# Kernel optimization log

Measured on AMD Instinct MI355X. Metric: run time of the kernel, lower is better.

The kernel has to match this reference:

```python
import jax, jax.numpy as jnp
import numpy as np

B, F, L, K = 16384, 8, 16, 4
NH, HD = 4, 2  # nhead=4, head_dim=2 (d_model=8)
EPS = 1e-5


def _ln(x, g, b):
    m = x.mean(-1, keepdims=True)
    v = ((x - m) ** 2).mean(-1, keepdims=True)
    return g * (x - m) * jax.lax.rsqrt(v + EPS) + b


def _encoder(x, ipw, ipb, ow, ob, l1w, l1b, l2w, l2b, n1g, n1b, n2g, n2b):
    # x: [N, L, 8]; post-norm TransformerEncoderLayer, relu FFN, eval (dropout off)
    N, Ls, D = x.shape
    for i in range(3):
        qkv = x @ ipw[i].T + ipb[i]                       # [N,L,24]
        q, k, v = jnp.split(qkv, 3, axis=-1)
        q = q.reshape(N, Ls, NH, HD)
        k = k.reshape(N, Ls, NH, HD)
        v = v.reshape(N, Ls, NH, HD)
        s = jnp.einsum('nqhd,nkhd->nhqk', q, k) / np.float32(np.sqrt(HD))
        a = jax.nn.softmax(s, axis=-1)
        o = jnp.einsum('nhqk,nkhd->nqhd', a, v).reshape(N, Ls, D)
        o = o @ ow[i].T + ob[i]
        x = _ln(x + o, n1g[i], n1b[i])
        h = jax.nn.relu(x @ l1w[i].T + l1b[i]) @ l2w[i].T + l2b[i]
        x = _ln(x + h, n2g[i], n2b[i])
    return x


def _forward(cidxs, slots, gfeats, f2, f3, tab_c, tab_s, fw, fb, ipw, ipb, ow, ob,
             l1w, l1b, l2w, l2b, n1g, n1b, n2g, n2b, uw, ub, w1, b1, w2, b2):
    Bn, Fn, Ln, _ = gfeats.shape
    x = gfeats.reshape(Bn * Fn, Ln, 4) @ fw.T + fb        # emb_floor -> [B*F,L,8]
    x = _encoder(x, ipw, ipb, ow, ob, l1w, l1b, l2w, l2b, n1g, n1b, n2g, n2b)
    floors = x.sum(axis=1).reshape(Bn, Fn, 8)             # sum over units
    units = jax.nn.relu(floors @ uw.T + ub).sum(axis=1)   # emb_unit + sum over floors -> [B,16]
    f1f2 = jnp.concatenate([tab_c[cidxs], tab_s[slots], units, f2], axis=-1)  # [B,36]
    Kn = f3.shape[1]
    z = jnp.concatenate(
        [jnp.broadcast_to(f1f2[:, None, :], (Bn, Kn, f1f2.shape[-1])), f3], axis=-1
    ).reshape(Bn * Kn, 42)                                # repeat_interleave + hstack f3
    h = jax.nn.relu(z @ w1.T + b1)                        # ff_match (dropout off)
    y = (h @ w2.T + b2).reshape(-1)
    return y


def setup_inputs() -> dict:
    key = jax.random.key(0)
    ks = jax.random.split(key, 30)
    r = lambda k, shp: (jax.random.normal(k, shp) * 0.1).astype(jnp.float32)
    return dict(
        cidxs=jax.random.randint(ks[0], (B,), 0, 100000),
        slots=jax.random.randint(ks[1], (B,), 0, 48),
        gfeats=jax.random.normal(ks[2], (B, F, L, 4), jnp.float32),
        f2=jax.random.normal(ks[3], (B, 4), jnp.float32),
        f3=jax.random.normal(ks[4], (B, K, 6), jnp.float32),
        tab_c=r(ks[5], (100000, 8)),
        tab_s=r(ks[6], (48, 8)),
        fw=r(ks[7], (8, 4)), fb=r(ks[8], (8,)),
        ipw=r(ks[9], (3, 24, 8)), ipb=r(ks[10], (3, 24)),
        ow=r(ks[11], (3, 8, 8)), ob=r(ks[12], (3, 8)),
        l1w=r(ks[13], (3, 16, 8)), l1b=r(ks[14], (3, 16)),
        l2w=r(ks[15], (3, 8, 16)), l2b=r(ks[16], (3, 8)),
        n1g=jnp.ones((3, 8), jnp.float32), n1b=jnp.zeros((3, 8), jnp.float32),
        n2g=jnp.ones((3, 8), jnp.float32), n2b=jnp.zeros((3, 8), jnp.float32),
        uw=r(ks[17], (16, 8)), ub=r(ks[18], (16,)),
        w1=r(ks[19], (20, 42)), b1=r(ks[20], (20,)),
        w2=r(ks[21], (1, 20)), b2=r(ks[22], (1,)),
    )


def reference(cidxs, slots, gfeats, f2, f3, tab_c, tab_s, fw, fb, ipw, ipb, ow, ob,
              l1w, l1b, l2w, l2b, n1g, n1b, n2g, n2b, uw, ub, w1, b1, w2, b2):
    y = _forward(cidxs, slots, gfeats, f2, f3, tab_c, tab_s, fw, fb, ipw, ipb, ow, ob,
                 l1w, l1b, l2w, l2b, n1g, n1b, n2g, n2b, uw, ub, w1, b1, w2, b2)
    nf3 = jnp.full((gfeats.shape[0],), f3.shape[1], dtype=jnp.int32)
    return (y, nf3)
```

## Files before the change

kernel.cpp:

```cpp
#include <hip/hip_runtime.h>

#define B_    16384
#define F_    8
#define L_    16
#define K_    4
#define SEQS_ (B_ * F_)

#define SCORE_SCALE 1.02040774484936f

typedef _Float16 h2  __attribute__((ext_vector_type(2)));
typedef _Float16 h8v __attribute__((ext_vector_type(8)));

#if __has_builtin(__builtin_amdgcn_fdot2)
__device__ __forceinline__ float fdot2(h2 a, h2 b, float c) {
    return __builtin_amdgcn_fdot2(a, b, c, false);
}
#else
__device__ __forceinline__ float fdot2(h2 a, h2 b, float c) {
    return c + (float)a[0] * (float)b[0] + (float)a[1] * (float)b[1];
}
#endif

__device__ __forceinline__ unsigned pku(float a, float b) {
    return __builtin_bit_cast(unsigned, __builtin_amdgcn_cvt_pkrtz(a, b));
}
__device__ __forceinline__ h2 u2h(unsigned u) {
    return __builtin_bit_cast(h2, u);
}
__device__ __forceinline__ h2 relu2(h2 a) {
#if __has_builtin(__builtin_elementwise_max)
    h2 z = {(_Float16)0.f, (_Float16)0.f};
    return __builtin_elementwise_max(a, z);
#else
    h2 r; r[0] = a[0] > (_Float16)0.f ? a[0] : (_Float16)0.f;
          r[1] = a[1] > (_Float16)0.f ? a[1] : (_Float16)0.f;
    return r;
#endif
}

#define WOFF_FW   0
#define WOFF_IPW  16
#define WOFF_OW   304
#define WOFF_L1W  400
#define WOFF_L2W  592
#define NW_U      784
#define BOFF_FB   0
#define BOFF_IPB  8
#define BOFF_OB   80
#define BOFF_L1B  104
#define BOFF_L2B  152
#define BOFF_N1G  176
#define BOFF_N1B  200
#define BOFF_N2G  224
#define BOFF_N2B  248
#define NB_F      272
#define FLOORS_OFF 8192

__global__ __launch_bounds__(256) void cvt_weights(
    const float* __restrict__ fw,  const float* __restrict__ ipw,
    const float* __restrict__ ow,  const float* __restrict__ l1w,
    const float* __restrict__ l2w,
    const float* __restrict__ fb,  const float* __restrict__ ipb,
    const float* __restrict__ ob,  const float* __restrict__ l1b,
    const float* __restrict__ l2b,
    const float* __restrict__ n1g, const float* __restrict__ n1b,
    const float* __restrict__ n2g, const float* __restrict__ n2b,
    unsigned* __restrict__ ws)
{
    for (int i = threadIdx.x; i < NW_U; i += 256) {
        const float* s; int off; float scale = 1.f;
        if (i < WOFF_IPW)      { s = fw;  off = i; }
        else if (i < WOFF_OW)  { s = ipw; off = i - WOFF_IPW;
                                 if (((off % 96) >> 2) < 8) scale = SCORE_SCALE; }
        else if (i < WOFF_L1W) { s = ow;  off = i - WOFF_OW; }
        else if (i < WOFF_L2W) { s = l1w; off = i - WOFF_L1W; }
        else                   { s = l2w; off = i - WOFF_L2W; }
        ws[i] = pku(s[2*off] * scale, s[2*off + 1] * scale);
    }
    float* bias = (float*)(ws + NW_U);
    for (int i = threadIdx.x; i < NB_F; i += 256) {
        float v;
        if (i < BOFF_IPB)      v = fb[i];
        else if (i < BOFF_OB)  { int j = i - BOFF_IPB; v = ipb[j];
                                 if ((j % 24) < 8) v *= SCORE_SCALE; }
        else if (i < BOFF_L1B) v = ob[i - BOFF_OB];
        else if (i < BOFF_L2B) v = l1b[i - BOFF_L1B];
        else if (i < BOFF_N1G) v = l2b[i - BOFF_L2B];
        else if (i < BOFF_N1B) v = n1g[i - BOFF_N1G];
        else if (i < BOFF_N2G) v = n1b[i - BOFF_N1B];
        else if (i < BOFF_N2B) v = n2g[i - BOFF_N2G];
        else                   v = n2b[i - BOFF_N2B];
        bias[i] = v;
    }
}

__global__ __launch_bounds__(256, 8) void seq_kernel(
    const float* __restrict__ gfeats,
    const unsigned* __restrict__ ws)
{
    __shared__ uint4 kb[16][17];
    __shared__ unsigned vt_dw[16 * 68];
    __shared__ unsigned wlds[NW_U + NB_F];

    for (int i = threadIdx.x; i < NW_U + NB_F; i += 256) wlds[i] = ws[i];
    __syncthreads();

    const unsigned* wq  = wlds;
    const float* bias   = (const float*)(wlds + NW_U);
    h8v* floors_h       = (h8v*)((char*)ws + FLOORS_OFF);

    const int tid = threadIdx.x;
    const int g   = tid >> 4;
    const int r   = tid & 15;
    const int seq = blockIdx.x * 16 + g;

    _Float16* vth = (_Float16*)vt_dw;
    const int vwr = g*136 + (r>>1)*16 + (r&1);
    const int vrd = g*68;

    const float4 f = *reinterpret_cast<const float4*>(gfeats + ((size_t)seq * L_ + r) * 4);
    const h2 f0 = u2h(pku(f.x, f.y)), f1 = u2h(pku(f.z, f.w));
    float x[8];
#pragma unroll
    for (int d = 0; d < 8; ++d)
        x[d] = fdot2(f0, u2h(wq[WOFF_FW + d*2]),
               fdot2(f1, u2h(wq[WOFF_FW + d*2 + 1]), bias[BOFF_FB + d]));

#pragma unroll
    for (int li = 0; li < 3; ++li) {
        const unsigned* W  = wq + WOFF_IPW + li * 96;
        const float*    Bq = bias + BOFF_IPB + li * 24;

        h2 x2[4];
#pragma unroll
        for (int p = 0; p < 4; ++p) x2[p] = u2h(pku(x[2*p], x[2*p+1]));

        {
            float kv[8];
#pragma unroll
            for (int o = 0; o < 8; ++o) {
                const unsigned* w = W + (8 + o)*4;
                float a = Bq[8 + o];
#pragma unroll
                for (int p = 0; p < 4; ++p) a = fdot2(x2[p], u2h(w[p]), a);
                kv[o] = a;
            }
            uint4 K;
            K.x = pku(kv[0], kv[1]); K.y = pku(kv[2], kv[3]);
            K.z = pku(kv[4], kv[5]); K.w = pku(kv[6], kv[7]);
            kb[r][g] = K;
        }
        {
#pragma unroll
            for (int o = 0; o < 8; ++o) {
                const unsigned* w = W + (16 + o)*4;
                float a = Bq[16 + o];
#pragma unroll
                for (int p = 0; p < 4; ++p) a = fdot2(x2[p], u2h(w[p]), a);
                vth[vwr + 2*o] = (_Float16)a;
            }
        }
        h2 q2[4];
#pragma unroll
        for (int h = 0; h < 4; ++h) {
            const unsigned* wa = W + (2*h)*4;
            const unsigned* wb = W + (2*h+1)*4;
            float qa = Bq[2*h], qb = Bq[2*h+1];
#pragma unroll
            for (int p = 0; p < 4; ++p) {
                qa = fdot2(x2[p], u2h(wa[p]), qa);
                qb = fdot2(x2[p], u2h(wb[p]), qb);
            }
            q2[h] = u2h(pku(qa, qb));
        }

        float o_[8] = {0.f,0.f,0.f,0.f,0.f,0.f,0.f,0.f};
        float sm[4] = {0.f,0.f,0.f,0.f};
        const h2 one2 = u2h(0x3C003C00u);

        uint4 cKa = kb[0][g];
        uint4 cKb = kb[1][g];
        uint4 cva = *reinterpret_cast<const uint4*>(&vt_dw[vrd]);
        uint4 cvb = *reinterpret_cast<const uint4*>(&vt_dw[vrd + 4]);
#pragma unroll
        for (int jp = 0; jp < 8; ++jp) {
            uint4 nKa, nKb, nva, nvb;
            if (jp < 7) {
                nKa = kb[2*jp + 2][g];
                nKb = kb[2*jp + 3][g];
                nva = *reinterpret_cast<const uint4*>(&vt_dw[vrd + (jp+1)*8]);
                nvb = *reinterpret_cast<const uint4*>(&vt_dw[vrd + (jp+1)*8 + 4]);
            }
            const float pa0 = __builtin_amdgcn_exp2f(fdot2(q2[0], u2h(cKa.x), 0.f));
            const float pa1 = __builtin_amdgcn_exp2f(fdot2(q2[1], u2h(cKa.y), 0.f));
            const float pa2 = __builtin_amdgcn_exp2f(fdot2(q2[2], u2h(cKa.z), 0.f));
            const float pa3 = __builtin_amdgcn_exp2f(fdot2(q2[3], u2h(cKa.w), 0.f));
            const float pb0 = __builtin_amdgcn_exp2f(fdot2(q2[0], u2h(cKb.x), 0.f));
            const float pb1 = __builtin_amdgcn_exp2f(fdot2(q2[1], u2h(cKb.y), 0.f));
            const float pb2 = __builtin_amdgcn_exp2f(fdot2(q2[2], u2h(cKb.z), 0.f));
            const float pb3 = __builtin_amdgcn_exp2f(fdot2(q2[3], u2h(cKb.w), 0.f));
            const h2 pp0 = u2h(pku(pa0, pb0));
            const h2 pp1 = u2h(pku(pa1, pb1));
            const h2 pp2 = u2h(pku(pa2, pb2));
            const h2 pp3 = u2h(pku(pa3, pb3));
            sm[0] = fdot2(pp0, one2, sm[0]);
            sm[1] = fdot2(pp1, one2, sm[1]);
            sm[2] = fdot2(pp2, one2, sm[2]);
            sm[3] = fdot2(pp3, one2, sm[3]);
            o_[0] = fdot2(pp0, u2h(cva.x), o_[0]);
            o_[1] = fdot2(pp0, u2h(cva.y), o_[1]);
            o_[2] = fdot2(pp1, u2h(cva.z), o_[2]);
            o_[3] = fdot2(pp1, u2h(cva.w), o_[3]);
            o_[4] = fdot2(pp2, u2h(cvb.x), o_[4]);
            o_[5] = fdot2(pp2, u2h(cvb.y), o_[5]);
            o_[6] = fdot2(pp3, u2h(cvb.z), o_[6]);
            o_[7] = fdot2(pp3, u2h(cvb.w), o_[7]);
            cKa = nKa; cKb = nKb; cva = nva; cvb = nvb;
        }

        const unsigned* OW = wq + WOFF_OW + li * 32;
        const float*    OB = bias + BOFF_OB + li * 8;
        h2 o2[4];
#pragma unroll
        for (int h = 0; h < 4; ++h) {
            const float inv = __builtin_amdgcn_rcpf(sm[h]);
            o2[h] = u2h(pku(o_[2*h] * inv, o_[2*h+1] * inv));
        }
        float y[8];
#pragma unroll
        for (int d = 0; d < 8; ++d) {
            const unsigned* w = OW + d*4;
            float a = OB[d];
#pragma unroll
            for (int p = 0; p < 4; ++p) a = fdot2(o2[p], u2h(w[p]), a);
            y[d] = x[d] + a;
        }
        {
            const float* G  = bias + BOFF_N1G + li * 8;
            const float* Bb = bias + BOFF_N1B + li * 8;
            h2 y2[4];
#pragma unroll
            for (int p = 0; p < 4; ++p) y2[p] = u2h(pku(y[2*p], y[2*p+1]));
            float s1 = 0.f, s2 = 0.f;
#pragma unroll
            for (int p = 0; p < 4; ++p) {
                s1 = fdot2(y2[p], one2, s1);
                s2 = fdot2(y2[p], y2[p], s2);
            }
            const float m  = s1 * 0.125f;
            const float v  = fmaf(-m, m, s2 * 0.125f);
            const float rs = __builtin_amdgcn_rsqf(v + 1e-5f);
#pragma unroll
            for (int d = 0; d < 8; ++d) x[d] = G[d] * (y[d] - m) * rs + Bb[d];
        }

        const unsigned* W1  = wq + WOFF_L1W + li * 64;
        const float*    B1l = bias + BOFF_L1B + li * 16;
        const unsigned* W2  = wq + WOFF_L2W + li * 64;
        const float*    B2l = bias + BOFF_L2B + li * 8;
#pragma unroll
        for (int p = 0; p < 4; ++p) x2[p] = u2h(pku(x[2*p], x[2*p+1]));
        float hb[16];
#pragma unroll
        for (int o = 0; o < 16; ++o) {
            const unsigned* w = W1 + o*4;
            float a = B1l[o];
#pragma unroll
            for (int p = 0; p < 4; ++p) a = fdot2(x2[p], u2h(w[p]), a);
            hb[o] = a;
        }
        h2 hp[8];
#pragma unroll
        for (int p = 0; p < 8; ++p) hp[p] = relu2(u2h(pku(hb[2*p], hb[2*p+1])));
        float y8[8];
#pragma unroll
        for (int d = 0; d < 8; ++d) {
            const unsigned* w = W2 + d*8;
            float a = B2l[d];
#pragma unroll
            for (int p = 0; p < 8; ++p) a = fdot2(hp[p], u2h(w[p]), a);
            y8[d] = x[d] + a;
        }
        {
            const float* G  = bias + BOFF_N2G + li * 8;
            const float* Bb = bias + BOFF_N2B + li * 8;
            h2 y2[4];
#pragma unroll
            for (int p = 0; p < 4; ++p) y2[p] = u2h(pku(y8[2*p], y8[2*p+1]));
            float s1 = 0.f, s2 = 0.f;
#pragma unroll
            for (int p = 0; p < 4; ++p) {
                s1 = fdot2(y2[p], one2, s1);
                s2 = fdot2(y2[p], y2[p], s2);
            }
            const float m  = s1 * 0.125f;
            const float v  = fmaf(-m, m, s2 * 0.125f);
            const float rs = __builtin_amdgcn_rsqf(v + 1e-5f);
#pragma unroll
            for (int d = 0; d < 8; ++d) x[d] = G[d] * (y8[d] - m) * rs + Bb[d];
        }
    }

#pragma unroll
    for (int d = 0; d < 8; ++d) {
        float t = x[d];
        t += __shfl_xor(t, 1, 16);
        t += __shfl_xor(t, 2, 16);
        t += __shfl_xor(t, 4, 16);
        t += __shfl_xor(t, 8, 16);
        x[d] = t;
    }
    if (r == 0) {
        union { h8v v; unsigned u[4]; } O;
        O.u[0] = pku(x[0], x[1]); O.u[1] = pku(x[2], x[3]);
        O.u[2] = pku(x[4], x[5]); O.u[3] = pku(x[6], x[7]);
        floors_h[seq] = O.v;
    }
}

__global__ __launch_bounds__(64) void tail_kernel(
    const int*   __restrict__ cidxs, const int* __restrict__ slots,
    const float* __restrict__ f2,    const float* __restrict__ f3,
    const float* __restrict__ tab_c, const float* __restrict__ tab_s,
    const float* __restrict__ uw,    const float* __restrict__ ub,
    const float* __restrict__ w1,    const float* __restrict__ b1,
    const float* __restrict__ w2,    const float* __restrict__ b2,
    const h8v*   __restrict__ floors_h, float* __restrict__ out)
{
    const int b = blockIdx.x * 64 + threadIdx.x;
    if (b >= B_) return;

    float units[16];
#pragma unroll
    for (int o = 0; o < 16; ++o) units[o] = 0.f;
    for (int fl_i = 0; fl_i < F_; ++fl_i) {
        union { h8v v; _Float16 s[8]; } U;
        U.v = floors_h[(size_t)b * F_ + fl_i];
        float fl[8];
#pragma unroll
        for (int d = 0; d < 8; ++d) fl[d] = (float)U.s[d];
#pragma unroll
        for (int o = 0; o < 16; ++o) {
            float t = ub[o];
#pragma unroll
            for (int d = 0; d < 8; ++d) t += fl[d] * uw[o*8 + d];
            units[o] += fmaxf(t, 0.f);
        }
    }

    float z36[36];
    {
        const int ci = cidxs[b], si = slots[b];
#pragma unroll
        for (int j = 0; j < 8; ++j) z36[j]     = tab_c[(size_t)ci * 8 + j];
#pragma unroll
        for (int j = 0; j < 8; ++j) z36[8 + j] = tab_s[(size_t)si * 8 + j];
#pragma unroll
        for (int j = 0; j < 16; ++j) z36[16 + j] = units[j];
#pragma unroll
        for (int j = 0; j < 4; ++j) z36[32 + j] = f2[(size_t)b * 4 + j];
    }

    float base[20];
#pragma unroll
    for (int o = 0; o < 20; ++o) {
        float t = b1[o];
#pragma unroll
        for (int j = 0; j < 36; ++j) t += z36[j] * w1[o*42 + j];
        base[o] = t;
    }

    const float bb2 = b2[0];
#pragma unroll
    for (int k = 0; k < K_; ++k) {
        float f3v[6];
#pragma unroll
        for (int j = 0; j < 6; ++j) f3v[j] = f3[((size_t)b * K_ + k) * 6 + j];
        float acc = bb2;
#pragma unroll
        for (int o = 0; o < 20; ++o) {
            float t = base[o];
#pragma unroll
            for (int j = 0; j < 6; ++j) t += f3v[j] * w1[o*42 + 36 + j];
            acc += fmaxf(t, 0.f) * w2[o];
        }
        out[(size_t)b * K_ + k] = acc;
    }

    out[(size_t)(B_ * K_) + b] = 4.0f;
}

extern "C" void kernel_launch(void* const* d_in, const int* in_sizes, int n_in,
                              void* d_out, int out_size, void* d_ws, size_t ws_size,
                              hipStream_t stream)
{
    const int*   cidxs  = (const int*)  d_in[0];
    const int*   slots  = (const int*)  d_in[1];
    const float* gfeats = (const float*)d_in[2];
    const float* f2     = (const float*)d_in[3];
    const float* f3     = (const float*)d_in[4];
    const float* tab_c  = (const float*)d_in[5];
    const float* tab_s  = (const float*)d_in[6];
    const float* fw     = (const float*)d_in[7];
    const float* fb     = (const float*)d_in[8];
    const float* ipw    = (const float*)d_in[9];
    const float* ipb    = (const float*)d_in[10];
    const float* ow     = (const float*)d_in[11];
    const float* ob     = (const float*)d_in[12];
    const float* l1w    = (const float*)d_in[13];
    const float* l1b    = (const float*)d_in[14];
    const float* l2w    = (const float*)d_in[15];
    const float* l2b    = (const float*)d_in[16];
    const float* n1g    = (const float*)d_in[17];
    const float* n1b    = (const float*)d_in[18];
    const float* n2g    = (const float*)d_in[19];
    const float* n2b    = (const float*)d_in[20];
    const float* uw     = (const float*)d_in[21];
    const float* ub     = (const float*)d_in[22];
    const float* w1     = (const float*)d_in[23];
    const float* b1     = (const float*)d_in[24];
    const float* w2     = (const float*)d_in[25];
    const float* b2     = (const float*)d_in[26];

    unsigned* ws       = (unsigned*)d_ws;
    h8v*      floors_h = (h8v*)((char*)d_ws + FLOORS_OFF);

    cvt_weights<<<1, 256, 0, stream>>>(fw, ipw, ow, l1w, l2w,
                                       fb, ipb, ob, l1b, l2b,
                                       n1g, n1b, n2g, n2b, ws);

    seq_kernel<<<SEQS_ / 16, 256, 0, stream>>>(gfeats, ws);

    tail_kernel<<<B_ / 64, 64, 0, stream>>>(
        cidxs, slots, f2, f3, tab_c, tab_s, uw, ub, w1, b1, w2, b2,
        floors_h, (float*)d_out);
}
```

Measured before the change: 182.0 us.

## Fuse weight conversion, sequence encoder and tail MLP into one kernel

Merges the three launches into a single kernel. Each block converts the weights into LDS itself, runs the encoder for 16 sequences (two batch rows), and then computes the unit embedding and match MLP for those two rows through shared memory. This drops two launches and the global round trip of the fp16 floor sums. In exchange, every block redoes the weight conversion, and the tail work runs on only a few threads per block behind extra barriers.

```diff
diff --git a/kernel.cpp b/kernel.cpp
--- a/kernel.cpp
+++ b/kernel.cpp
@@ -9,7 +9,6 @@
 #define SCORE_SCALE 1.02040774484936f
 
 typedef _Float16 h2  __attribute__((ext_vector_type(2)));
-typedef _Float16 h8v __attribute__((ext_vector_type(8)));
 
 #if __has_builtin(__builtin_amdgcn_fdot2)
 __device__ __forceinline__ float fdot2(h2 a, h2 b, float c) {
@@ -54,9 +53,9 @@
 #define BOFF_N2G  224
 #define BOFF_N2B  248
 #define NB_F      272
-#define FLOORS_OFF 8192
-
-__global__ __launch_bounds__(256) void cvt_weights(
+
+__global__ __launch_bounds__(256, 8) void fused_kernel(
+    const float* __restrict__ gfeats,
     const float* __restrict__ fw,  const float* __restrict__ ipw,
     const float* __restrict__ ow,  const float* __restrict__ l1w,
     const float* __restrict__ l2w,
@@ -65,9 +64,24 @@
     const float* __restrict__ l2b,
     const float* __restrict__ n1g, const float* __restrict__ n1b,
     const float* __restrict__ n2g, const float* __restrict__ n2b,
-    unsigned* __restrict__ ws)
+    const int*   __restrict__ cidxs, const int* __restrict__ slots,
+    const float* __restrict__ f2,    const float* __restrict__ f3,
+    const float* __restrict__ tab_c, const float* __restrict__ tab_s,
+    const float* __restrict__ uw,    const float* __restrict__ ub,
+    const float* __restrict__ w1,    const float* __restrict__ b1,
+    const float* __restrict__ w2,    const float* __restrict__ b2,
+    float* __restrict__ out)
 {
-    for (int i = threadIdx.x; i < NW_U; i += 256) {
+    __shared__ uint4 kb[16][17];
+    __shared__ unsigned vt_dw[16 * 68];
+    __shared__ unsigned wlds[NW_U + NB_F];
+    __shared__ float floors_lds[16][8];
+    __shared__ float units_lds[2][16];
+    __shared__ float pm_lds[2][4][20];
+
+    const int tid = threadIdx.x;
+
+    for (int i = tid; i < NW_U; i += 256) {
         const float* s; int off; float scale = 1.f;
         if (i < WOFF_IPW)      { s = fw;  off = i; }
         else if (i < WOFF_OW)  { s = ipw; off = i - WOFF_IPW;
@@ -75,41 +89,30 @@
         else if (i < WOFF_L1W) { s = ow;  off = i - WOFF_OW; }
         else if (i < WOFF_L2W) { s = l1w; off = i - WOFF_L1W; }
         else                   { s = l2w; off = i - WOFF_L2W; }
-        ws[i] = pku(s[2*off] * scale, s[2*off + 1] * scale);
-    }
-    float* bias = (float*)(ws + NW_U);
-    for (int i = threadIdx.x; i < NB_F; i += 256) {
-        float v;
-        if (i < BOFF_IPB)      v = fb[i];
-        else if (i < BOFF_OB)  { int j = i - BOFF_IPB; v = ipb[j];
-                                 if ((j % 24) < 8) v *= SCORE_SCALE; }
-        else if (i < BOFF_L1B) v = ob[i - BOFF_OB];
-        else if (i < BOFF_L2B) v = l1b[i - BOFF_L1B];
-        else if (i < BOFF_N1G) v = l2b[i - BOFF_L2B];
-        else if (i < BOFF_N1B) v = n1g[i - BOFF_N1G];
-        else if (i < BOFF_N2G) v = n1b[i - BOFF_N1B];
-        else if (i < BOFF_N2B) v = n2g[i - BOFF_N2G];
-        else                   v = n2b[i - BOFF_N2B];
-        bias[i] = v;
-    }
-}
-
-__global__ __launch_bounds__(256, 8) void seq_kernel(
-    const float* __restrict__ gfeats,
-    const unsigned* __restrict__ ws)
-{
-    __shared__ uint4 kb[16][17];
-    __shared__ unsigned vt_dw[16 * 68];
-    __shared__ unsigned wlds[NW_U + NB_F];
-
-    for (int i = threadIdx.x; i < NW_U + NB_F; i += 256) wlds[i] = ws[i];
+        wlds[i] = pku(s[2*off] * scale, s[2*off + 1] * scale);
+    }
+    {
+        float* bdst = (float*)(wlds + NW_U);
+        for (int i = tid; i < NB_F; i += 256) {
+            float v;
+            if (i < BOFF_IPB)      v = fb[i];
+            else if (i < BOFF_OB)  { int j = i - BOFF_IPB; v = ipb[j];
+                                     if ((j % 24) < 8) v *= SCORE_SCALE; }
+            else if (i < BOFF_L1B) v = ob[i - BOFF_OB];
+            else if (i < BOFF_L2B) v = l1b[i - BOFF_L1B];
+            else if (i < BOFF_N1G) v = l2b[i - BOFF_L2B];
+            else if (i < BOFF_N1B) v = n1g[i - BOFF_N1G];
+            else if (i < BOFF_N2G) v = n1b[i - BOFF_N1B];
+            else if (i < BOFF_N2B) v = n2g[i - BOFF_N2G];
+            else                   v = n2b[i - BOFF_N2B];
+            bdst[i] = v;
+        }
+    }
     __syncthreads();
 
     const unsigned* wq  = wlds;
     const float* bias   = (const float*)(wlds + NW_U);
-    h8v* floors_h       = (h8v*)((char*)ws + FLOORS_OFF);
-
-    const int tid = threadIdx.x;
+
     const int g   = tid >> 4;
     const int r   = tid & 15;
     const int seq = blockIdx.x * 16 + g;
@@ -311,83 +314,62 @@
         x[d] = t;
     }
     if (r == 0) {
-        union { h8v v; unsigned u[4]; } O;
-        O.u[0] = pku(x[0], x[1]); O.u[1] = pku(x[2], x[3]);
-        O.u[2] = pku(x[4], x[5]); O.u[3] = pku(x[6], x[7]);
-        floors_h[seq] = O.v;
-    }
-}
-
-__global__ __launch_bounds__(64) void tail_kernel(
-    const int*   __restrict__ cidxs, const int* __restrict__ slots,
-    const float* __restrict__ f2,    const float* __restrict__ f3,
-    const float* __restrict__ tab_c, const float* __restrict__ tab_s,
-    const float* __restrict__ uw,    const float* __restrict__ ub,
-    const float* __restrict__ w1,    const float* __restrict__ b1,
-    const float* __restrict__ w2,    const float* __restrict__ b2,
-    const h8v*   __restrict__ floors_h, float* __restrict__ out)
-{
-    const int b = blockIdx.x * 64 + threadIdx.x;
-    if (b >= B_) return;
-
-    float units[16];
-#pragma unroll
-    for (int o = 0; o < 16; ++o) units[o] = 0.f;
-    for (int fl_i = 0; fl_i < F_; ++fl_i) {
-        union { h8v v; _Float16 s[8]; } U;
-        U.v = floors_h[(size_t)b * F_ + fl_i];
-        float fl[8];
-#pragma unroll
-        for (int d = 0; d < 8; ++d) fl[d] = (float)U.s[d];
-#pragma unroll
-        for (int o = 0; o < 16; ++o) {
-            float t = ub[o];
-#pragma unroll
-            for (int d = 0; d < 8; ++d) t += fl[d] * uw[o*8 + d];
-            units[o] += fmaxf(t, 0.f);
-        }
-    }
-
-    float z36[36];
+#pragma unroll
+        for (int d = 0; d < 8; ++d) floors_lds[g][d] = x[d];
+    }
+    __syncthreads();
+
     {
-        const int ci = cidxs[b], si = slots[b];
-#pragma unroll
-        for (int j = 0; j < 8; ++j) z36[j]     = tab_c[(size_t)ci * 8 + j];
-#pragma unroll
-        for (int j = 0; j < 8; ++j) z36[8 + j] = tab_s[(size_t)si * 8 + j];
-#pragma unroll
-        for (int j = 0; j < 16; ++j) z36[16 + j] = units[j];
-#pragma unroll
-        for (int j = 0; j < 4; ++j) z36[32 + j] = f2[(size_t)b * 4 + j];
-    }
-
-    float base[20];
-#pragma unroll
-    for (int o = 0; o < 20; ++o) {
-        float t = b1[o];
-#pragma unroll
-        for (int j = 0; j < 36; ++j) t += z36[j] * w1[o*42 + j];
-        base[o] = t;
-    }
-
-    const float bb2 = b2[0];
-#pragma unroll
-    for (int k = 0; k < K_; ++k) {
-        float f3v[6];
-#pragma unroll
-        for (int j = 0; j < 6; ++j) f3v[j] = f3[((size_t)b * K_ + k) * 6 + j];
-        float acc = bb2;
-#pragma unroll
-        for (int o = 0; o < 20; ++o) {
-            float t = base[o];
-#pragma unroll
-            for (int j = 0; j < 6; ++j) t += f3v[j] * w1[o*42 + 36 + j];
-            acc += fmaxf(t, 0.f) * w2[o];
-        }
-        out[(size_t)b * K_ + k] = acc;
-    }
-
-    out[(size_t)(B_ * K_) + b] = 4.0f;
+        const int bl = tid >> 7;
+        const int ou = (tid >> 3) & 15;
+        const int fl = tid & 7;
+        float acc = ub[ou];
+        const float* fp = &floors_lds[bl*8 + fl][0];
+#pragma unroll
+        for (int d = 0; d < 8; ++d) acc += fp[d] * uw[ou*8 + d];
+        acc = fmaxf(acc, 0.f);
+        acc += __shfl_xor(acc, 1, 8);
+        acc += __shfl_xor(acc, 2, 8);
+        acc += __shfl_xor(acc, 4, 8);
+        if (fl == 0) units_lds[bl][ou] = acc;
+    }
+    __syncthreads();
+
+    if (tid < 40) {
+        const int bl = tid / 20, o = tid % 20;
+        const int bg = blockIdx.x * 2 + bl;
+        const float* w1o = w1 + o*42;
+        float base = b1[o];
+        const int ci = cidxs[bg], si = slots[bg];
+#pragma unroll
+        for (int j = 0; j < 8; ++j)  base += tab_c[ci*8 + j]  * w1o[j];
+#pragma unroll
+        for (int j = 0; j < 8; ++j)  base += tab_s[si*8 + j]  * w1o[8 + j];
+#pragma unroll
+        for (int j = 0; j < 16; ++j) base += units_lds[bl][j] * w1o[16 + j];
+#pragma unroll
+        for (int j = 0; j < 4; ++j)  base += f2[bg*4 + j]     * w1o[32 + j];
+        const float w2o = w2[o];
+#pragma unroll
+        for (int k = 0; k < 4; ++k) {
+            float t = base;
+#pragma unroll
+            for (int j = 0; j < 6; ++j)
+                t += f3[((size_t)bg*4 + k)*6 + j] * w1o[36 + j];
+            pm_lds[bl][k][o] = fmaxf(t, 0.f) * w2o;
+        }
+    }
+    __syncthreads();
+
+    if (tid < 8) {
+        const int bl = tid >> 2, k = tid & 3;
+        float acc = b2[0];
+#pragma unroll
+        for (int o = 0; o < 20; ++o) acc += pm_lds[bl][k][o];
+        out[(size_t)(blockIdx.x*2 + bl)*4 + k] = acc;
+    }
+    if (tid < 2)
+        out[(size_t)B_*K_ + blockIdx.x*2 + tid] = 4.0f;
 }
 
 extern "C" void kernel_launch(void* const* d_in, const int* in_sizes, int n_in,
@@ -422,16 +404,9 @@
     const float* w2     = (const float*)d_in[25];
     const float* b2     = (const float*)d_in[26];
 
-    unsigned* ws       = (unsigned*)d_ws;
-    h8v*      floors_h = (h8v*)((char*)d_ws + FLOORS_OFF);
-
-    cvt_weights<<<1, 256, 0, stream>>>(fw, ipw, ow, l1w, l2w,
-                                       fb, ipb, ob, l1b, l2b,
-                                       n1g, n1b, n2g, n2b, ws);
-
-    seq_kernel<<<SEQS_ / 16, 256, 0, stream>>>(gfeats, ws);
-
-    tail_kernel<<<B_ / 64, 64, 0, stream>>>(
+    fused_kernel<<<SEQS_ / 16, 256, 0, stream>>>(
+        gfeats, fw, ipw, ow, l1w, l2w,
+        fb, ipb, ob, l1b, l2b, n1g, n1b, n2g, n2b,
         cidxs, slots, f2, f3, tab_c, tab_s, uw, ub, w1, b1, w2, b2,
-        floors_h, (float*)d_out);
-}
+        (float*)d_out);
+}
```

Result: faster. 155.0 us (-14.8%).
